# Optimization experiments

Hardware: AMD Instinct MI355X
Metric: run time of the kernel (lower is better)

Reference implementation:

```python
import jax, jax.numpy as jnp
import numpy as np

DMODEL = 65  # module-level constant in the source, used for both proj width and scale
DK = DQ = DV = 64
B, L = 8, 4096


def setup_inputs() -> dict:
    key = jax.random.key(0)
    ks = jax.random.split(key, 7)
    s = 1.0 / np.sqrt(DMODEL)
    return {
        "x":  jax.random.normal(ks[0], (B, L, DMODEL), dtype=jnp.float32),
        "Wq": jax.random.uniform(ks[1], (DMODEL, DQ), jnp.float32, -s, s),
        "bq": jax.random.uniform(ks[2], (DQ,), jnp.float32, -s, s),
        "Wk": jax.random.uniform(ks[3], (DMODEL, DK), jnp.float32, -s, s),
        "bk": jax.random.uniform(ks[4], (DK,), jnp.float32, -s, s),
        "Wv": jax.random.uniform(ks[5], (DMODEL, DV), jnp.float32, -s, s),
        "bv": jax.random.uniform(ks[6], (DV,), jnp.float32, -s, s),
    }


def reference(x, Wq, bq, Wk, bk, Wv, bv):
    # QKV projections (single head)
    q = x @ Wq + bq            # [B, L, DQ]
    k = x @ Wk + bk            # [B, L, DK]
    v = x @ Wv + bv            # [B, L, DV]
    # scaled dot-product scores; source scales by sqrt(dmodel)=sqrt(65)
    scores = jnp.einsum("bqd,bkd->bqk", q, k) / (DMODEL ** 0.5)  # [B, L, L]
    # causal mask (intended semantics of the source's tril-based masked_fill)
    causal = jnp.tril(jnp.ones((L, L), dtype=bool))
    scores = jnp.where(causal, scores, jnp.float32(-jnp.inf))
    probs = jax.nn.softmax(scores, axis=-1)  # dropout omitted (eval mode)
    return probs @ v           # [B, L, DV]
```

## Files before the change

### kernel.cpp

```cpp
#include <hip/hip_runtime.h>
#include <hip/hip_bf16.h>

#define B_  8
#define L_  4096
#define DH  64

typedef __attribute__((ext_vector_type(8)))  __bf16 bf16x8;
typedef __attribute__((ext_vector_type(16))) float  f32x16;
typedef __attribute__((ext_vector_type(4)))  float  f32x4;
typedef __attribute__((ext_vector_type(8)))  unsigned short u16x8;

#define QW_OFF  0u
#define KW_OFF  2097152u
#define VP_OFF  4194304u
#define OP_OFF  6291456u
#define LP_OFFB 46137344u

__global__ __launch_bounds__(256) void qkv_proj(
    const float* __restrict__ x,
    const float* __restrict__ Wq, const float* __restrict__ bq,
    const float* __restrict__ Wk, const float* __restrict__ bk,
    const float* __restrict__ Wv, const float* __restrict__ bv,
    unsigned short* __restrict__ qo,
    unsigned short* __restrict__ Kp,
    unsigned short* __restrict__ Vp)
{
    __shared__ __align__(16) unsigned short xs[64 * 104];
    __shared__ __align__(16) unsigned short wt[64 * 104];
    __shared__ __align__(16) unsigned short bounce[64 * 64];
    __shared__ float bsm[64];

    const int tid = threadIdx.x;
    const int r0  = blockIdx.x * 64;
    const int bb  = r0 >> 12;
    const int l0  = r0 & 4095;

    {
        const u16x8 z = {0,0,0,0,0,0,0,0};
        for (int i = tid; i < (64 * 104) / 8; i += 256) {
            ((u16x8*)xs)[i] = z;  ((u16x8*)wt)[i] = z;
        }
    }
    __syncthreads();

    for (int i = tid; i < 64 * 65; i += 256) {
        const int row = i / 65, col = i - row * 65;
        __hip_bfloat16 v = __float2bfloat16(x[(size_t)r0 * 65 + i]);
        xs[row * 104 + col] = *(unsigned short*)&v;
    }

    const float* Wp[3] = {Wq, Wk, Wv};
    const float* bp[3] = {bq, bk, bv};

    const int w = tid >> 6, lane = tid & 63, li = lane & 15, lg = lane >> 4;
    const int rb = w * 16;

#pragma unroll
    for (int p = 0; p < 3; ++p) {
        __syncthreads();
        for (int i = tid; i < 65 * 64; i += 256) {
            const int k = i >> 6, cc = i & 63;
            __hip_bfloat16 v = __float2bfloat16(Wp[p][i]);
            wt[cc * 104 + k] = *(unsigned short*)&v;
        }
        if (tid < 64) bsm[tid] = bp[p][tid];
        __syncthreads();

        f32x4 acc[4];
#pragma unroll
        for (int j = 0; j < 4; ++j) {
            const float bv_ = bsm[j * 16 + li];
            acc[j] = (f32x4){bv_, bv_, bv_, bv_};
        }
#pragma unroll
        for (int ks = 0; ks < 3; ++ks) {
            const bf16x8 a = __builtin_bit_cast(bf16x8,
                *(const u16x8*)&xs[(rb + li) * 104 + ks * 32 + 8 * lg]);
#pragma unroll
            for (int j = 0; j < 4; ++j) {
                const bf16x8 bf = __builtin_bit_cast(bf16x8,
                    *(const u16x8*)&wt[(j * 16 + li) * 104 + ks * 32 + 8 * lg]);
                acc[j] = __builtin_amdgcn_mfma_f32_16x16x32_bf16(a, bf, acc[j], 0, 0, 0);
            }
        }

        const float scale = (p == 0) ? (1.4426950408889634f / 8.06225774829855f) : 1.0f;
#pragma unroll
        for (int j = 0; j < 4; ++j)
#pragma unroll
            for (int r = 0; r < 4; ++r) {
                __hip_bfloat16 hv = __float2bfloat16(acc[j][r] * scale);
                bounce[(rb + lg * 4 + r) * 64 + j * 16 + li] = *(unsigned short*)&hv;
            }
        __syncthreads();

        if (p == 0) {
            const int row = tid >> 2, col = (tid & 3) * 16;
            unsigned short* op = qo + (size_t)(r0 + row) * 64 + col;
            *(u16x8*)op       = *(const u16x8*)&bounce[row * 64 + col];
            *(u16x8*)(op + 8) = *(const u16x8*)&bounce[row * 64 + col + 8];
        } else if (p == 1) {
#pragma unroll
            for (int e = 0; e < 2; ++e) {
                const int pi = tid * 2 + e;
                const int row = pi >> 3, s = pi & 7;
                const int l = l0 + row;
                const u16x8 piece = *(const u16x8*)&bounce[row * 64 + ((s ^ (row & 7)) << 3)];
                *(u16x8*)(Kp + (size_t)(bb * 128 + (l >> 5)) * 2048 + (l & 31) * 64 + s * 8) = piece;
            }
        } else {
#pragma unroll
            for (int e = 0; e < 2; ++e) {
                const int pi = tid * 2 + e;
                const int t32 = pi >> 8, rem = pi & 255;
                const int dv = rem >> 2, cp = rem & 3;
                const int u = cp ^ ((dv >> 1) & 3);
                const int m = u >> 1, h = u & 1;
                u16x8 piece;
#pragma unroll
                for (int j = 0; j < 8; ++j) {
                    const int kv = m * 16 + h * 4 + (j & 3) + 8 * (j >> 2);
                    piece[j] = bounce[(t32 * 32 + kv) * 64 + dv];
                }
                *(u16x8*)(Vp + (size_t)(bb * 128 + (l0 >> 5) + t32) * 2048 + dv * 32 + cp * 8) = piece;
            }
        }
    }
}

__global__ __launch_bounds__(256, 3) void attn(
    const unsigned short* __restrict__ Q,
    const unsigned short* __restrict__ Kp,
    const unsigned short* __restrict__ Vp,
    float* __restrict__ O,
    unsigned short* __restrict__ Op,
    float* __restrict__ Lp)
{
    __shared__ __align__(16) unsigned short SM[2][8192];

    const int tid  = threadIdx.x;
    const int w    = tid >> 6;
    const int lane = tid & 63;
    const int li32 = lane & 31;
    const int h    = lane >> 5;

    const int b = blockIdx.x & 7;
    const int p = 143 - (blockIdx.x >> 3);
    int g = 0;
    while (2 * (g + 1) * (g + 2) <= p) ++g;
    const int id2 = p - 2 * g * (g + 1);
    const int qq  = id2 / (g + 1);
    const int qb  = 4 * g + qq;
    const int c   = id2 - qq * (g + 1);

    const int q0    = qb * 128;
    const int kv0   = c << 9;
    const int kvend = (kv0 + 512 < q0 + 128) ? kv0 + 512 : q0 + 128;
    const int ntl   = (kvend - kv0) >> 6;
    const int q0w   = q0 + w * 32;
    const int q     = q0w + li32;

    const size_t base = (size_t)b * L_ * DH;
    const unsigned short* KpB = Kp + ((size_t)(b * 128) + (kv0 >> 5)) * 2048;
    const unsigned short* VpB = Vp + ((size_t)(b * 128) + (kv0 >> 5)) * 2048;

    bf16x8 qf[4];
#pragma unroll
    for (int ks = 0; ks < 4; ++ks)
        qf[ks] = __builtin_bit_cast(bf16x8,
            *(const u16x8*)(Q + base + (size_t)q * DH + ks * 16 + h * 8));

    u16x8 ou;
#pragma unroll
    for (int i = 0; i < 8; ++i) ou[i] = 0x3F80;
    const bf16x8 ones = __builtin_bit_cast(bf16x8, ou);

    f32x16 o0, o1, l_acc;
#pragma unroll
    for (int r = 0; r < 16; ++r) { o0[r] = 0.0f; o1[r] = 0.0f; l_acc[r] = 0.0f; }

    auto stage_t = [&](int buf, int t) {
        const unsigned short* ksrc = KpB + (size_t)t * 4096 + w * 512 + lane * 8;
        const unsigned short* vsrc = VpB + (size_t)t * 4096 + w * 512 + lane * 8;
        unsigned short* kdst = &SM[buf][0]    + w * 512;
        unsigned short* vdst = &SM[buf][4096] + w * 512;
#pragma unroll
        for (int j2 = 0; j2 < 2; ++j2) {
            __builtin_amdgcn_global_load_lds(
                (const __attribute__((address_space(1))) void*)(ksrc + j2 * 2048),
                (__attribute__((address_space(3))) void*)(kdst + j2 * 2048), 16, 0, 0);
            __builtin_amdgcn_global_load_lds(
                (const __attribute__((address_space(1))) void*)(vsrc + j2 * 2048),
                (__attribute__((address_space(3))) void*)(vdst + j2 * 2048), 16, 0, 0);
        }
    };

    stage_t(0, 0);
    if (ntl > 1) stage_t(1, 1);

    for (int t = 0; t < ntl; ++t) {
        if (t + 1 < ntl) { asm volatile("s_waitcnt vmcnt(4)" ::: "memory"); }
        else             { asm volatile("s_waitcnt vmcnt(0)" ::: "memory"); }
        __builtin_amdgcn_s_barrier();

        const int kvb = kv0 + t * 64;
        const unsigned short* SMp = &SM[t & 1][0];

        if (kvb <= q0w + 31) {
#pragma unroll
            for (int sub = 0; sub < 2; ++sub) {
                const int kvbs = kvb + sub * 32;
                if (sub == 1 && kvbs > q0w + 31) break;
                const int soff = sub * 2048;

                f32x16 s;
#pragma unroll
                for (int r = 0; r < 16; ++r) s[r] = -8.0f;
#pragma unroll
                for (int ks = 0; ks < 4; ++ks) {
                    const bf16x8 kf = __builtin_bit_cast(bf16x8,
                        *(const u16x8*)&SMp[soff + li32 * 64 +
                                            ((((ks << 1) | h) ^ (li32 & 7)) << 3)]);
                    s = __builtin_amdgcn_mfma_f32_32x32x16_bf16(kf, qf[ks], s, 0, 0, 0);
                }

                if (kvbs + 31 > q0w) {
#pragma unroll
                    for (int r = 0; r < 16; ++r) {
                        const int kv = kvbs + (r & 3) + ((r >> 2) << 3) + (h << 2);
                        s[r] = (kv > q) ? -1e30f : s[r];
                    }
                }

#pragma unroll
                for (int r = 0; r < 16; ++r) s[r] = __builtin_amdgcn_exp2f(s[r]);

                bf16x8 pf0, pf1;
#pragma unroll
                for (int i = 0; i < 8; ++i) {
                    pf0[i] = (__bf16)s[i];
                    pf1[i] = (__bf16)s[8 + i];
                }

                l_acc = __builtin_amdgcn_mfma_f32_32x32x16_bf16(pf0, ones, l_acc, 0, 0, 0);
                l_acc = __builtin_amdgcn_mfma_f32_32x32x16_bf16(pf1, ones, l_acc, 0, 0, 0);

                {
                    const int dv = li32;
                    const int c0 = ((0 | h) ^ ((dv >> 1) & 3)) << 3;
                    const int c1 = ((2 | h) ^ ((dv >> 1) & 3)) << 3;
                    const bf16x8 v0 = __builtin_bit_cast(bf16x8,
                        *(const u16x8*)&SMp[4096 + soff + dv * 32 + c0]);
                    const bf16x8 v1 = __builtin_bit_cast(bf16x8,
                        *(const u16x8*)&SMp[4096 + soff + dv * 32 + c1]);
                    o0 = __builtin_amdgcn_mfma_f32_32x32x16_bf16(pf0, v0, o0, 0, 0, 0);
                    o0 = __builtin_amdgcn_mfma_f32_32x32x16_bf16(pf1, v1, o0, 0, 0, 0);
                }
                {
                    const int dv = 32 + li32;
                    const int c0 = ((0 | h) ^ ((dv >> 1) & 3)) << 3;
                    const int c1 = ((2 | h) ^ ((dv >> 1) & 3)) << 3;
                    const bf16x8 v0 = __builtin_bit_cast(bf16x8,
                        *(const u16x8*)&SMp[4096 + soff + dv * 32 + c0]);
                    const bf16x8 v1 = __builtin_bit_cast(bf16x8,
                        *(const u16x8*)&SMp[4096 + soff + dv * 32 + c1]);
                    o1 = __builtin_amdgcn_mfma_f32_32x32x16_bf16(pf0, v0, o1, 0, 0, 0);
                    o1 = __builtin_amdgcn_mfma_f32_32x32x16_bf16(pf1, v1, o1, 0, 0, 0);
                }
            }
        }

        __builtin_amdgcn_s_barrier();
        if (t + 2 < ntl) stage_t(t & 1, t + 2);
    }

    if (g == 0) {
#pragma unroll
        for (int r = 0; r < 16; ++r) {
            const int row = (r & 3) + ((r >> 2) << 3) + (h << 2);
            const float inv = 1.0f / l_acc[r];
            float* orow = O + ((size_t)b * L_ + q0w + row) * DH;
            orow[li32]      = o0[r] * inv;
            orow[32 + li32] = o1[r] * inv;
        }
    } else {
        const int idx = (b * 32 + qb) * 8 + c;
        unsigned short* po = Op + (size_t)idx * 8192;
        float* lp = Lp + (size_t)idx * 128;
#pragma unroll
        for (int r = 0; r < 16; ++r) {
            const int row = (r & 3) + ((r >> 2) << 3) + (h << 2);
            __hip_bfloat16 h0 = __float2bfloat16(o0[r]);
            __hip_bfloat16 h1 = __float2bfloat16(o1[r]);
            po[(w * 32 + row) * 64 + li32]      = *(unsigned short*)&h0;
            po[(w * 32 + row) * 64 + 32 + li32] = *(unsigned short*)&h1;
            if (li32 == 0) lp[w * 32 + row] = l_acc[r];
        }
    }
}

__global__ __launch_bounds__(256) void merge(
    const unsigned short* __restrict__ Op,
    const float* __restrict__ Lp,
    float* __restrict__ O)
{
    const int b  = blockIdx.x & 7;
    const int qb = 4 + (blockIdx.x >> 3);
    const int nc = (qb >> 2) + 1;

    const int row = threadIdx.x >> 1;
    const int c0  = (threadIdx.x & 1) * 32;
    const int idx0 = (b * 32 + qb) * 8;

    float acc[32];
#pragma unroll
    for (int j = 0; j < 32; ++j) acc[j] = 0.0f;
    float Lr = 0.0f;

    for (int cc = 0; cc < nc; ++cc) {
        Lr += Lp[(size_t)(idx0 + cc) * 128 + row];
        const unsigned short* pp = Op + (size_t)(idx0 + cc) * 8192 + row * 64 + c0;
#pragma unroll
        for (int j8 = 0; j8 < 4; ++j8) {
            const u16x8 a = *(const u16x8*)(pp + j8 * 8);
#pragma unroll
            for (int j = 0; j < 8; ++j) {
                const unsigned int ua = ((unsigned int)a[j]) << 16;
                acc[j8 * 8 + j] += __builtin_bit_cast(float, ua);
            }
        }
    }

    const float inv = 1.0f / Lr;
    float* out = O + ((size_t)b * L_ + qb * 128 + row) * DH + c0;
#pragma unroll
    for (int j4 = 0; j4 < 8; ++j4) {
        f32x4 v;
#pragma unroll
        for (int j = 0; j < 4; ++j) v[j] = acc[j4 * 4 + j] * inv;
        *(f32x4*)(out + j4 * 4) = v;
    }
}

extern "C" void kernel_launch(void* const* d_in, const int* in_sizes, int n_in,
                              void* d_out, int out_size, void* d_ws, size_t ws_size,
                              hipStream_t stream)
{
    const float* x  = (const float*)d_in[0];
    const float* Wq = (const float*)d_in[1];
    const float* bq = (const float*)d_in[2];
    const float* Wk = (const float*)d_in[3];
    const float* bk = (const float*)d_in[4];
    const float* Wv = (const float*)d_in[5];
    const float* bv = (const float*)d_in[6];

    unsigned short* ws16 = (unsigned short*)d_ws;
    unsigned short* qw  = ws16 + QW_OFF;
    unsigned short* kp  = ws16 + KW_OFF;
    unsigned short* vp  = ws16 + VP_OFF;
    unsigned short* Opp = ws16 + OP_OFF;
    float* Lp = (float*)((char*)d_ws + LP_OFFB);

    qkv_proj<<<512, 256, 0, stream>>>(x, Wq, bq, Wk, bk, Wv, bv, qw, kp, vp);
    attn<<<1152, 256, 0, stream>>>(qw, kp, vp, (float*)d_out, Opp, Lp);
    merge<<<224, 256, 0, stream>>>(Opp, Lp, (float*)d_out);
}
```

Measured before the change: 53.46 us.

## Precompute transposed bf16 weights once and widen merge kernel parallelism

A small prep kernel converts and transposes Wq/Wk/Wv to bf16 once, with the Q scale folded into the weights and bias. The 512 projection blocks then read these fragments straight from global memory instead of each re-converting the weights into shared memory behind extra barriers. Separately, the merge kernel spreads each row over 8 threads with 8 columns each and uses 896 blocks instead of 224, for more parallelism and fewer registers per thread. The cost is an extra kernel launch, and the B operand of the MFMA is now read from global/L2 instead of LDS.

Result: slower. 60.64 us (+13.4%).

```diff
diff --git a/kernel.cpp b/kernel.cpp
--- a/kernel.cpp
+++ b/kernel.cpp
@@ -15,20 +15,42 @@
 #define VP_OFF  4194304u
 #define OP_OFF  6291456u
 #define LP_OFFB 46137344u
-
-__global__ __launch_bounds__(256) void qkv_proj(
-    const float* __restrict__ x,
+#define WT_OFFB 47185920u
+#define BS_OFFB 47222784u
+
+__global__ __launch_bounds__(256) void prep(
     const float* __restrict__ Wq, const float* __restrict__ bq,
     const float* __restrict__ Wk, const float* __restrict__ bk,
     const float* __restrict__ Wv, const float* __restrict__ bv,
+    unsigned short* __restrict__ WT, float* __restrict__ bias_s)
+{
+    const int p = blockIdx.x;
+    const float* W  = (p == 0) ? Wq : (p == 1) ? Wk : Wv;
+    const float* bb = (p == 0) ? bq : (p == 1) ? bk : bv;
+    const float scale = (p == 0) ? (1.4426950408889634f / 8.06225774829855f) : 1.0f;
+
+    const int c  = threadIdx.x & 63;
+    const int kq = threadIdx.x >> 6;
+#pragma unroll
+    for (int kk = 0; kk < 24; ++kk) {
+        const int k = kq * 24 + kk;
+        const float v = (k < 65) ? W[k * 64 + c] * scale : 0.0f;
+        __hip_bfloat16 h = __float2bfloat16(v);
+        WT[(p * 64 + c) * 96 + k] = *(unsigned short*)&h;
+    }
+    if (threadIdx.x < 64) bias_s[p * 64 + threadIdx.x] = bb[threadIdx.x] * scale;
+}
+
+__global__ __launch_bounds__(256) void qkv_proj(
+    const float* __restrict__ x,
+    const unsigned short* __restrict__ WT,
+    const float* __restrict__ bias_s,
     unsigned short* __restrict__ qo,
     unsigned short* __restrict__ Kp,
     unsigned short* __restrict__ Vp)
 {
     __shared__ __align__(16) unsigned short xs[64 * 104];
-    __shared__ __align__(16) unsigned short wt[64 * 104];
     __shared__ __align__(16) unsigned short bounce[64 * 64];
-    __shared__ float bsm[64];
 
     const int tid = threadIdx.x;
     const int r0  = blockIdx.x * 64;
@@ -37,9 +59,7 @@
 
     {
         const u16x8 z = {0,0,0,0,0,0,0,0};
-        for (int i = tid; i < (64 * 104) / 8; i += 256) {
-            ((u16x8*)xs)[i] = z;  ((u16x8*)wt)[i] = z;
-        }
+        for (int i = tid; i < (64 * 104) / 8; i += 256) ((u16x8*)xs)[i] = z;
     }
     __syncthreads();
 
@@ -49,27 +69,16 @@
         xs[row * 104 + col] = *(unsigned short*)&v;
     }
 
-    const float* Wp[3] = {Wq, Wk, Wv};
-    const float* bp[3] = {bq, bk, bv};
-
     const int w = tid >> 6, lane = tid & 63, li = lane & 15, lg = lane >> 4;
     const int rb = w * 16;
+    __syncthreads();
 
 #pragma unroll
     for (int p = 0; p < 3; ++p) {
-        __syncthreads();
-        for (int i = tid; i < 65 * 64; i += 256) {
-            const int k = i >> 6, cc = i & 63;
-            __hip_bfloat16 v = __float2bfloat16(Wp[p][i]);
-            wt[cc * 104 + k] = *(unsigned short*)&v;
-        }
-        if (tid < 64) bsm[tid] = bp[p][tid];
-        __syncthreads();
-
         f32x4 acc[4];
 #pragma unroll
         for (int j = 0; j < 4; ++j) {
-            const float bv_ = bsm[j * 16 + li];
+            const float bv_ = bias_s[p * 64 + j * 16 + li];
             acc[j] = (f32x4){bv_, bv_, bv_, bv_};
         }
 #pragma unroll
@@ -79,17 +88,18 @@
 #pragma unroll
             for (int j = 0; j < 4; ++j) {
                 const bf16x8 bf = __builtin_bit_cast(bf16x8,
-                    *(const u16x8*)&wt[(j * 16 + li) * 104 + ks * 32 + 8 * lg]);
+                    *(const u16x8*)(WT + (size_t)(p * 64 + j * 16 + li) * 96
+                                    + ks * 32 + 8 * lg));
                 acc[j] = __builtin_amdgcn_mfma_f32_16x16x32_bf16(a, bf, acc[j], 0, 0, 0);
             }
         }
 
-        const float scale = (p == 0) ? (1.4426950408889634f / 8.06225774829855f) : 1.0f;
+        __syncthreads();
 #pragma unroll
         for (int j = 0; j < 4; ++j)
 #pragma unroll
             for (int r = 0; r < 4; ++r) {
-                __hip_bfloat16 hv = __float2bfloat16(acc[j][r] * scale);
+                __hip_bfloat16 hv = __float2bfloat16(acc[j][r]);
                 bounce[(rb + lg * 4 + r) * 64 + j * 16 + li] = *(unsigned short*)&hv;
             }
         __syncthreads();
@@ -304,42 +314,38 @@
     const float* __restrict__ Lp,
     float* __restrict__ O)
 {
-    const int b  = blockIdx.x & 7;
-    const int qb = 4 + (blockIdx.x >> 3);
-    const int nc = (qb >> 2) + 1;
-
-    const int row = threadIdx.x >> 1;
-    const int c0  = (threadIdx.x & 1) * 32;
+    const int b     = blockIdx.x & 7;
+    const int rest  = blockIdx.x >> 3;
+    const int qb    = 4 + (rest >> 2);
+    const int slice = rest & 3;
+    const int nc    = (qb >> 2) + 1;
+
+    const int row = slice * 32 + (threadIdx.x >> 3);
+    const int cg  = (threadIdx.x & 7) * 8;
     const int idx0 = (b * 32 + qb) * 8;
 
-    float acc[32];
-#pragma unroll
-    for (int j = 0; j < 32; ++j) acc[j] = 0.0f;
+    float acc[8];
+#pragma unroll
+    for (int j = 0; j < 8; ++j) acc[j] = 0.0f;
     float Lr = 0.0f;
 
     for (int cc = 0; cc < nc; ++cc) {
         Lr += Lp[(size_t)(idx0 + cc) * 128 + row];
-        const unsigned short* pp = Op + (size_t)(idx0 + cc) * 8192 + row * 64 + c0;
-#pragma unroll
-        for (int j8 = 0; j8 < 4; ++j8) {
-            const u16x8 a = *(const u16x8*)(pp + j8 * 8);
-#pragma unroll
-            for (int j = 0; j < 8; ++j) {
-                const unsigned int ua = ((unsigned int)a[j]) << 16;
-                acc[j8 * 8 + j] += __builtin_bit_cast(float, ua);
-            }
+        const u16x8 a = *(const u16x8*)(Op + (size_t)(idx0 + cc) * 8192 + row * 64 + cg);
+#pragma unroll
+        for (int j = 0; j < 8; ++j) {
+            const unsigned int ua = ((unsigned int)a[j]) << 16;
+            acc[j] += __builtin_bit_cast(float, ua);
         }
     }
 
     const float inv = 1.0f / Lr;
-    float* out = O + ((size_t)b * L_ + qb * 128 + row) * DH + c0;
-#pragma unroll
-    for (int j4 = 0; j4 < 8; ++j4) {
-        f32x4 v;
-#pragma unroll
-        for (int j = 0; j < 4; ++j) v[j] = acc[j4 * 4 + j] * inv;
-        *(f32x4*)(out + j4 * 4) = v;
-    }
+    float* out = O + ((size_t)b * L_ + qb * 128 + row) * DH + cg;
+    f32x4 v0, v1;
+#pragma unroll
+    for (int j = 0; j < 4; ++j) { v0[j] = acc[j] * inv; v1[j] = acc[4 + j] * inv; }
+    *(f32x4*)out       = v0;
+    *(f32x4*)(out + 4) = v1;
 }
 
 extern "C" void kernel_launch(void* const* d_in, const int* in_sizes, int n_in,
@@ -360,8 +366,11 @@
     unsigned short* vp  = ws16 + VP_OFF;
     unsigned short* Opp = ws16 + OP_OFF;
     float* Lp = (float*)((char*)d_ws + LP_OFFB);
-
-    qkv_proj<<<512, 256, 0, stream>>>(x, Wq, bq, Wk, bk, Wv, bv, qw, kp, vp);
+    unsigned short* WT = (unsigned short*)((char*)d_ws + WT_OFFB);
+    float* bias_s = (float*)((char*)d_ws + BS_OFFB);
+
+    prep<<<3, 256, 0, stream>>>(Wq, bq, Wk, bk, Wv, bv, WT, bias_s);
+    qkv_proj<<<512, 256, 0, stream>>>(x, WT, bias_s, qw, kp, vp);
     attn<<<1152, 256, 0, stream>>>(qw, kp, vp, (float*)d_out, Opp, Lp);
-    merge<<<224, 256, 0, stream>>>(Opp, Lp, (float*)d_out);
-}
+    merge<<<896, 256, 0, stream>>>(Opp, Lp, (float*)d_out);
+}
```

## Load K/V fragments directly from global into registers, dropping LDS staging

Applied to the files above, without the earlier changes.

The attention kernel no longer stages K and V tiles through double-buffered shared memory with block barriers. Each wave now loads its K and V MFMA fragments straight from global memory into registers, prefetching the next 32-key sub-tile, and loops only over the sub-tiles it needs up to its diagonal. The projection kernel drops the XOR swizzle from the packed K/V layouts, since there are no LDS bank conflicts left to avoid, and the occupancy hint on the launch bounds is removed. The aim is to remove LDS traffic and barrier stalls. The cost is that the four waves each fetch the same K/V data redundantly from L2/global, and register pressure rises.

Measured after the change: 92.94 us. +73.9%, slower.

```diff
diff --git a/kernel.cpp b/kernel.cpp
--- a/kernel.cpp
+++ b/kernel.cpp
@@ -105,7 +105,7 @@
                 const int pi = tid * 2 + e;
                 const int row = pi >> 3, s = pi & 7;
                 const int l = l0 + row;
-                const u16x8 piece = *(const u16x8*)&bounce[row * 64 + ((s ^ (row & 7)) << 3)];
+                const u16x8 piece = *(const u16x8*)&bounce[row * 64 + (s << 3)];
                 *(u16x8*)(Kp + (size_t)(bb * 128 + (l >> 5)) * 2048 + (l & 31) * 64 + s * 8) = piece;
             }
         } else {
@@ -114,12 +114,11 @@
                 const int pi = tid * 2 + e;
                 const int t32 = pi >> 8, rem = pi & 255;
                 const int dv = rem >> 2, cp = rem & 3;
-                const int u = cp ^ ((dv >> 1) & 3);
-                const int m = u >> 1, h = u & 1;
+                const int m = cp >> 1, hh = cp & 1;
                 u16x8 piece;
 #pragma unroll
                 for (int j = 0; j < 8; ++j) {
-                    const int kv = m * 16 + h * 4 + (j & 3) + 8 * (j >> 2);
+                    const int kv = m * 16 + hh * 4 + (j & 3) + 8 * (j >> 2);
                     piece[j] = bounce[(t32 * 32 + kv) * 64 + dv];
                 }
                 *(u16x8*)(Vp + (size_t)(bb * 128 + (l0 >> 5) + t32) * 2048 + dv * 32 + cp * 8) = piece;
@@ -128,7 +127,7 @@
     }
 }
 
-__global__ __launch_bounds__(256, 3) void attn(
+__global__ __launch_bounds__(256) void attn(
     const unsigned short* __restrict__ Q,
     const unsigned short* __restrict__ Kp,
     const unsigned short* __restrict__ Vp,
@@ -136,8 +135,6 @@
     unsigned short* __restrict__ Op,
     float* __restrict__ Lp)
 {
-    __shared__ __align__(16) unsigned short SM[2][8192];
-
     const int tid  = threadIdx.x;
     const int w    = tid >> 6;
     const int lane = tid & 63;
@@ -156,13 +153,17 @@
     const int q0    = qb * 128;
     const int kv0   = c << 9;
     const int kvend = (kv0 + 512 < q0 + 128) ? kv0 + 512 : q0 + 128;
-    const int ntl   = (kvend - kv0) >> 6;
+    const int nsub  = (kvend - kv0) >> 5;
     const int q0w   = q0 + w * 32;
     const int q     = q0w + li32;
+    const int sdiag = (q0w - kv0) >> 5;
+    const int ns    = (sdiag + 1 < nsub) ? sdiag + 1 : nsub;
 
     const size_t base = (size_t)b * L_ * DH;
-    const unsigned short* KpB = Kp + ((size_t)(b * 128) + (kv0 >> 5)) * 2048;
-    const unsigned short* VpB = Vp + ((size_t)(b * 128) + (kv0 >> 5)) * 2048;
+    const unsigned short* kbase =
+        Kp + ((size_t)(b * 128) + (kv0 >> 5)) * 2048 + li32 * 64 + h * 8;
+    const unsigned short* vbase =
+        Vp + ((size_t)(b * 128) + (kv0 >> 5)) * 2048 + li32 * 32 + h * 8;
 
     bf16x8 qf[4];
 #pragma unroll
@@ -179,99 +180,63 @@
 #pragma unroll
     for (int r = 0; r < 16; ++r) { o0[r] = 0.0f; o1[r] = 0.0f; l_acc[r] = 0.0f; }
 
-    auto stage_t = [&](int buf, int t) {
-        const unsigned short* ksrc = KpB + (size_t)t * 4096 + w * 512 + lane * 8;
-        const unsigned short* vsrc = VpB + (size_t)t * 4096 + w * 512 + lane * 8;
-        unsigned short* kdst = &SM[buf][0]    + w * 512;
-        unsigned short* vdst = &SM[buf][4096] + w * 512;
-#pragma unroll
-        for (int j2 = 0; j2 < 2; ++j2) {
-            __builtin_amdgcn_global_load_lds(
-                (const __attribute__((address_space(1))) void*)(ksrc + j2 * 2048),
-                (__attribute__((address_space(3))) void*)(kdst + j2 * 2048), 16, 0, 0);
-            __builtin_amdgcn_global_load_lds(
-                (const __attribute__((address_space(1))) void*)(vsrc + j2 * 2048),
-                (__attribute__((address_space(3))) void*)(vdst + j2 * 2048), 16, 0, 0);
-        }
-    };
-
-    stage_t(0, 0);
-    if (ntl > 1) stage_t(1, 1);
-
-    for (int t = 0; t < ntl; ++t) {
-        if (t + 1 < ntl) { asm volatile("s_waitcnt vmcnt(4)" ::: "memory"); }
-        else             { asm volatile("s_waitcnt vmcnt(0)" ::: "memory"); }
-        __builtin_amdgcn_s_barrier();
-
-        const int kvb = kv0 + t * 64;
-        const unsigned short* SMp = &SM[t & 1][0];
-
-        if (kvb <= q0w + 31) {
-#pragma unroll
-            for (int sub = 0; sub < 2; ++sub) {
-                const int kvbs = kvb + sub * 32;
-                if (sub == 1 && kvbs > q0w + 31) break;
-                const int soff = sub * 2048;
-
-                f32x16 s;
-#pragma unroll
-                for (int r = 0; r < 16; ++r) s[r] = -8.0f;
-#pragma unroll
-                for (int ks = 0; ks < 4; ++ks) {
-                    const bf16x8 kf = __builtin_bit_cast(bf16x8,
-                        *(const u16x8*)&SMp[soff + li32 * 64 +
-                                            ((((ks << 1) | h) ^ (li32 & 7)) << 3)]);
-                    s = __builtin_amdgcn_mfma_f32_32x32x16_bf16(kf, qf[ks], s, 0, 0, 0);
-                }
-
-                if (kvbs + 31 > q0w) {
-#pragma unroll
-                    for (int r = 0; r < 16; ++r) {
-                        const int kv = kvbs + (r & 3) + ((r >> 2) << 3) + (h << 2);
-                        s[r] = (kv > q) ? -1e30f : s[r];
-                    }
-                }
-
-#pragma unroll
-                for (int r = 0; r < 16; ++r) s[r] = __builtin_amdgcn_exp2f(s[r]);
-
-                bf16x8 pf0, pf1;
-#pragma unroll
-                for (int i = 0; i < 8; ++i) {
-                    pf0[i] = (__bf16)s[i];
-                    pf1[i] = (__bf16)s[8 + i];
-                }
-
-                l_acc = __builtin_amdgcn_mfma_f32_32x32x16_bf16(pf0, ones, l_acc, 0, 0, 0);
-                l_acc = __builtin_amdgcn_mfma_f32_32x32x16_bf16(pf1, ones, l_acc, 0, 0, 0);
-
-                {
-                    const int dv = li32;
-                    const int c0 = ((0 | h) ^ ((dv >> 1) & 3)) << 3;
-                    const int c1 = ((2 | h) ^ ((dv >> 1) & 3)) << 3;
-                    const bf16x8 v0 = __builtin_bit_cast(bf16x8,
-                        *(const u16x8*)&SMp[4096 + soff + dv * 32 + c0]);
-                    const bf16x8 v1 = __builtin_bit_cast(bf16x8,
-                        *(const u16x8*)&SMp[4096 + soff + dv * 32 + c1]);
-                    o0 = __builtin_amdgcn_mfma_f32_32x32x16_bf16(pf0, v0, o0, 0, 0, 0);
-                    o0 = __builtin_amdgcn_mfma_f32_32x32x16_bf16(pf1, v1, o0, 0, 0, 0);
-                }
-                {
-                    const int dv = 32 + li32;
-                    const int c0 = ((0 | h) ^ ((dv >> 1) & 3)) << 3;
-                    const int c1 = ((2 | h) ^ ((dv >> 1) & 3)) << 3;
-                    const bf16x8 v0 = __builtin_bit_cast(bf16x8,
-                        *(const u16x8*)&SMp[4096 + soff + dv * 32 + c0]);
-                    const bf16x8 v1 = __builtin_bit_cast(bf16x8,
-                        *(const u16x8*)&SMp[4096 + soff + dv * 32 + c1]);
-                    o1 = __builtin_amdgcn_mfma_f32_32x32x16_bf16(pf0, v0, o1, 0, 0, 0);
-                    o1 = __builtin_amdgcn_mfma_f32_32x32x16_bf16(pf1, v1, o1, 0, 0, 0);
-                }
-            }
-        }
-
-        __builtin_amdgcn_s_barrier();
-        if (t + 2 < ntl) stage_t(t & 1, t + 2);
+    u16x8 kf[4], vf[4];
+#pragma unroll
+    for (int ks = 0; ks < 4; ++ks) kf[ks] = *(const u16x8*)(kbase + ks * 16);
+    vf[0] = *(const u16x8*)(vbase);
+    vf[1] = *(const u16x8*)(vbase + 16);
+    vf[2] = *(const u16x8*)(vbase + 1024);
+    vf[3] = *(const u16x8*)(vbase + 1024 + 16);
+
+    for (int s = 0; s < ns; ++s) {
+        u16x8 kn[4], vn[4];
+        if (s + 1 < ns) {
+            const unsigned short* kb2 = kbase + (size_t)(s + 1) * 2048;
+            const unsigned short* vb2 = vbase + (size_t)(s + 1) * 2048;
+#pragma unroll
+            for (int ks = 0; ks < 4; ++ks) kn[ks] = *(const u16x8*)(kb2 + ks * 16);
+            vn[0] = *(const u16x8*)(vb2);
+            vn[1] = *(const u16x8*)(vb2 + 16);
+            vn[2] = *(const u16x8*)(vb2 + 1024);
+            vn[3] = *(const u16x8*)(vb2 + 1024 + 16);
+        }
+
+        f32x16 sa;
+#pragma unroll
+        for (int r = 0; r < 16; ++r) sa[r] = -8.0f;
+#pragma unroll
+        for (int ks = 0; ks < 4; ++ks)
+            sa = __builtin_amdgcn_mfma_f32_32x32x16_bf16(
+                __builtin_bit_cast(bf16x8, kf[ks]), qf[ks], sa, 0, 0, 0);
+
+        if (s == sdiag) {
+            const int kvbs = kv0 + s * 32;
+#pragma unroll
+            for (int r = 0; r < 16; ++r) {
+                const int kv = kvbs + (r & 3) + ((r >> 2) << 3) + (h << 2);
+                sa[r] = (kv > q) ? -1e30f : sa[r];
+            }
+        }
+
+#pragma unroll
+        for (int r = 0; r < 16; ++r) sa[r] = __builtin_amdgcn_exp2f(sa[r]);
+
+        bf16x8 pf0, pf1;
+#pragma unroll
+        for (int i = 0; i < 8; ++i) { pf0[i] = (__bf16)sa[i]; pf1[i] = (__bf16)sa[8 + i]; }
+
+        l_acc = __builtin_amdgcn_mfma_f32_32x32x16_bf16(pf0, ones, l_acc, 0, 0, 0);
+        l_acc = __builtin_amdgcn_mfma_f32_32x32x16_bf16(pf1, ones, l_acc, 0, 0, 0);
+
+        o0 = __builtin_amdgcn_mfma_f32_32x32x16_bf16(pf0, __builtin_bit_cast(bf16x8, vf[0]), o0, 0, 0, 0);
+        o0 = __builtin_amdgcn_mfma_f32_32x32x16_bf16(pf1, __builtin_bit_cast(bf16x8, vf[1]), o0, 0, 0, 0);
+        o1 = __builtin_amdgcn_mfma_f32_32x32x16_bf16(pf0, __builtin_bit_cast(bf16x8, vf[2]), o1, 0, 0, 0);
+        o1 = __builtin_amdgcn_mfma_f32_32x32x16_bf16(pf1, __builtin_bit_cast(bf16x8, vf[3]), o1, 0, 0, 0);
+
+        if (s + 1 < ns) {
+#pragma unroll
+            for (int i = 0; i < 4; ++i) { kf[i] = kn[i]; vf[i] = vn[i]; }
+        }
     }
 
     if (g == 0) {
```
